# Kernel tuning notes

Hardware: AMD Instinct MI355X
Metric: run time of the kernel (lower is better)

The kernel has to match this reference:

```python
import jax, jax.numpy as jnp
import numpy as np
from jax import lax


def setup_inputs() -> dict:
    key = jax.random.key(0)
    x = jax.random.normal(key, (16, 3, 1024, 1024), dtype=jnp.float32)
    return {"x": x, "kernel_size": 7}


def _box_conv(x, kernel, pad):
    # x: (B,1,H,W), kernel: (1,1,k,k); 'same' spatial conv
    return lax.conv_general_dilated(
        x, kernel,
        window_strides=(1, 1),
        padding=[(pad, pad), (pad, pad)],
        dimension_numbers=("NCHW", "OIHW", "NCHW"),
    )


def reference(x, kernel_size):
    k = kernel_size
    pad = k // 2
    # ConvertToLuminance: for 4D input, x.dim()==4 -> channel mean (not RGB weights)
    lum = jnp.mean(x, axis=1, keepdims=True)  # (B,1,H,W)
    kernel = jnp.ones((1, 1, k, k), dtype=x.dtype) / (k * k)
    mean = _box_conv(lum, kernel, pad)
    sqr_mean = _box_conv(lum * lum, kernel, pad)
    var = sqr_mean - mean * mean
    return var
```

## Files before the change

### kernel.cpp

```cpp
#include <hip/hip_runtime.h>

#define TILE 64
#define HALO 3
#define REG  (TILE + 2 * HALO)
#define LDSS (REG + 2)
#define H 1024
#define W 1024

__global__ __launch_bounds__(256)
void lvm_kernel(const float* __restrict__ x, float* __restrict__ out) {
    __shared__ float lum[REG][LDSS];
    __shared__ float hs1[REG][TILE];
    __shared__ float hs2[REG][TILE];

    const int b    = blockIdx.z;
    const int row0 = blockIdx.y * TILE - HALO;
    const int col0 = blockIdx.x * TILE - HALO;
    const int tid  = threadIdx.x;

    const float* xb = x + (size_t)b * 3 * H * W;

    for (int idx = tid; idx < REG * REG; idx += 256) {
        int r = idx / REG;
        int c = idx - r * REG;
        int gh = row0 + r, gw = col0 + c;
        float v = 0.0f;
        if (gh >= 0 && gh < H && gw >= 0 && gw < W) {
            size_t o = (size_t)gh * W + gw;
            v = (xb[o] + xb[o + (size_t)H * W] + xb[o + 2 * (size_t)H * W]) * (1.0f / 3.0f);
        }
        lum[r][c] = v;
    }
    __syncthreads();

    for (int idx = tid; idx < REG * TILE; idx += 256) {
        int r = idx >> 6;
        int c = idx & 63;
        float s1 = 0.0f, s2 = 0.0f;
#pragma unroll
        for (int j = 0; j < 7; ++j) {
            float v = lum[r][c + j];
            s1 += v;
            s2 += v * v;
        }
        hs1[r][c] = s1;
        hs2[r][c] = s2;
    }
    __syncthreads();

    const int oh0 = blockIdx.y * TILE;
    const int ow0 = blockIdx.x * TILE;
    float* ob = out + (size_t)b * H * W;
    for (int idx = tid; idx < TILE * TILE; idx += 256) {
        int r = idx >> 6;
        int c = idx & 63;
        float s1 = 0.0f, s2 = 0.0f;
#pragma unroll
        for (int j = 0; j < 7; ++j) {
            s1 += hs1[r + j][c];
            s2 += hs2[r + j][c];
        }
        float m   = s1 * (1.0f / 49.0f);
        float var = s2 * (1.0f / 49.0f) - m * m;
        ob[(size_t)(oh0 + r) * W + (ow0 + c)] = var;
    }
}

extern "C" void kernel_launch(void* const* d_in, const int* in_sizes, int n_in,
                              void* d_out, int out_size, void* d_ws, size_t ws_size,
                              hipStream_t stream) {
    const float* x = (const float*)d_in[0];
    float* out = (float*)d_out;
    dim3 grid(W / TILE, H / TILE, 16);
    lvm_kernel<<<grid, dim3(256), 0, stream>>>(x, out);
}
```

Measured before the change: 373.9 us.

## Stream full-width row strips with register ring buffer for vertical box sums

```diff
diff --git a/kernel.cpp b/kernel.cpp
--- a/kernel.cpp
+++ b/kernel.cpp
@@ -1,68 +1,91 @@
 #include <hip/hip_runtime.h>
 
-#define TILE 64
-#define HALO 3
-#define REG  (TILE + 2 * HALO)
-#define LDSS (REG + 2)
-#define H 1024
-#define W 1024
+#define Wd 1024
+#define Hd 1024
+#define SH 16
+#define ITER (SH + 6)
 
-__global__ __launch_bounds__(256)
-void lvm_kernel(const float* __restrict__ x, float* __restrict__ out) {
-    __shared__ float lum[REG][LDSS];
-    __shared__ float hs1[REG][TILE];
-    __shared__ float hs2[REG][TILE];
+__global__ __launch_bounds__(256, 4)
+void lvm_stream(const float* __restrict__ x, float* __restrict__ out) {
+    __shared__ __align__(16) float L[2][Wd + 8];
 
-    const int b    = blockIdx.z;
-    const int row0 = blockIdx.y * TILE - HALO;
-    const int col0 = blockIdx.x * TILE - HALO;
+    const int b    = blockIdx.y;
+    const int row0 = blockIdx.x * SH;
     const int tid  = threadIdx.x;
+    const int c0   = tid * 4;
 
-    const float* xb = x + (size_t)b * 3 * H * W;
+    const float* x0 = x + (size_t)b * 3 * Hd * Wd;
+    const float* x1 = x0 + (size_t)Hd * Wd;
+    const float* x2 = x1 + (size_t)Hd * Wd;
+    float*       ob = out + (size_t)b * Hd * Wd;
 
-    for (int idx = tid; idx < REG * REG; idx += 256) {
-        int r = idx / REG;
-        int c = idx - r * REG;
-        int gh = row0 + r, gw = col0 + c;
-        float v = 0.0f;
-        if (gh >= 0 && gh < H && gw >= 0 && gw < W) {
-            size_t o = (size_t)gh * W + gw;
-            v = (xb[o] + xb[o + (size_t)H * W] + xb[o + 2 * (size_t)H * W]) * (1.0f / 3.0f);
+    if (tid < 4) {
+        L[0][tid] = 0.f; L[0][Wd + 4 + tid] = 0.f;
+        L[1][tid] = 0.f; L[1][Wd + 4 + tid] = 0.f;
+    }
+
+    float4 ring1[7], ring2[7];
+
+#pragma unroll
+    for (int i = 0; i < ITER; ++i) {
+        const int ri = row0 - 3 + i;
+        float4 lum4 = make_float4(0.f, 0.f, 0.f, 0.f);
+        if (ri >= 0 && ri < Hd) {
+            size_t o = (size_t)ri * Wd + c0;
+            float4 a = *(const float4*)(x0 + o);
+            float4 g = *(const float4*)(x1 + o);
+            float4 c = *(const float4*)(x2 + o);
+            lum4.x = (a.x + g.x + c.x) * (1.f / 3.f);
+            lum4.y = (a.y + g.y + c.y) * (1.f / 3.f);
+            lum4.z = (a.z + g.z + c.z) * (1.f / 3.f);
+            lum4.w = (a.w + g.w + c.w) * (1.f / 3.f);
         }
-        lum[r][c] = v;
-    }
-    __syncthreads();
+        float* Lr = L[i & 1];
+        *(float4*)(Lr + 4 + c0) = lum4;
+        __syncthreads();
 
-    for (int idx = tid; idx < REG * TILE; idx += 256) {
-        int r = idx >> 6;
-        int c = idx & 63;
-        float s1 = 0.0f, s2 = 0.0f;
+        float4 va = *(const float4*)(Lr + c0);
+        float4 vb = *(const float4*)(Lr + c0 + 4);
+        float4 vc = *(const float4*)(Lr + c0 + 8);
+        float v1 = va.y, v2 = va.z, v3 = va.w;
+        float v4 = vb.x, v5 = vb.y, v6 = vb.z, v7 = vb.w;
+        float v8 = vc.x, v9 = vc.y, v10 = vc.z;
+
+        float s1a = v1 + v2 + v3 + v4 + v5 + v6 + v7;
+        float s1b = s1a - v1 + v8;
+        float s1c = s1b - v2 + v9;
+        float s1d = s1c - v3 + v10;
+
+        float q1 = v1 * v1, q2 = v2 * v2, q3 = v3 * v3, q4 = v4 * v4;
+        float q5 = v5 * v5, q6 = v6 * v6, q7 = v7 * v7, q8 = v8 * v8;
+        float q9 = v9 * v9, q10 = v10 * v10;
+        float s2a = q1 + q2 + q3 + q4 + q5 + q6 + q7;
+        float s2b = s2a - q1 + q8;
+        float s2c = s2b - q2 + q9;
+        float s2d = s2c - q3 + q10;
+
+        ring1[i % 7] = make_float4(s1a, s1b, s1c, s1d);
+        ring2[i % 7] = make_float4(s2a, s2b, s2c, s2d);
+
+        if (i >= 6) {
+            float4 t1 = ring1[0], t2 = ring2[0];
 #pragma unroll
-        for (int j = 0; j < 7; ++j) {
-            float v = lum[r][c + j];
-            s1 += v;
-            s2 += v * v;
+            for (int k = 1; k < 7; ++k) {
+                t1.x += ring1[k].x; t1.y += ring1[k].y;
+                t1.z += ring1[k].z; t1.w += ring1[k].w;
+                t2.x += ring2[k].x; t2.y += ring2[k].y;
+                t2.z += ring2[k].z; t2.w += ring2[k].w;
+            }
+            const float inv = 1.f / 49.f;
+            float4 r;
+            float mx = t1.x * inv, my = t1.y * inv, mz = t1.z * inv, mw = t1.w * inv;
+            r.x = t2.x * inv - mx * mx;
+            r.y = t2.y * inv - my * my;
+            r.z = t2.z * inv - mz * mz;
+            r.w = t2.w * inv - mw * mw;
+            const int ro = row0 + i - 6;
+            *(float4*)(ob + (size_t)ro * Wd + c0) = r;
         }
-        hs1[r][c] = s1;
-        hs2[r][c] = s2;
-    }
-    __syncthreads();
-
-    const int oh0 = blockIdx.y * TILE;
-    const int ow0 = blockIdx.x * TILE;
-    float* ob = out + (size_t)b * H * W;
-    for (int idx = tid; idx < TILE * TILE; idx += 256) {
-        int r = idx >> 6;
-        int c = idx & 63;
-        float s1 = 0.0f, s2 = 0.0f;
-#pragma unroll
-        for (int j = 0; j < 7; ++j) {
-            s1 += hs1[r + j][c];
-            s2 += hs2[r + j][c];
-        }
-        float m   = s1 * (1.0f / 49.0f);
-        float var = s2 * (1.0f / 49.0f) - m * m;
-        ob[(size_t)(oh0 + r) * W + (ow0 + c)] = var;
     }
 }
 
@@ -71,6 +94,6 @@
                               hipStream_t stream) {
     const float* x = (const float*)d_in[0];
     float* out = (float*)d_out;
-    dim3 grid(W / TILE, H / TILE, 16);
-    lvm_kernel<<<grid, dim3(256), 0, stream>>>(x, out);
+    dim3 grid(Hd / SH, 16);
+    lvm_stream<<<grid, dim3(256), 0, stream>>>(x, out);
 }
```

Result: faster. 302.3 us (-19.2%).
